# Performance work log

Hardware: AMD Instinct MI355X
Metric: run time of the kernel (lower is better)

Reference implementation:

```python
import jax, jax.numpy as jnp
import numpy as np

NUM_EXPERTS = 8
TOP_K = 2
HIDDEN = 1024
INTER = 4096
STD = 0.02


def setup_inputs() -> dict:
    key = jax.random.key(0)
    k0, k1, k2, k3 = jax.random.split(key, 4)
    hidden_states = jax.random.normal(k0, (2, 2048, HIDDEN), dtype=jnp.float32)
    gate_w = jax.random.normal(k1, (NUM_EXPERTS, HIDDEN), dtype=jnp.float32) * (HIDDEN ** -0.5)
    w1 = jax.random.normal(k2, (NUM_EXPERTS, INTER, HIDDEN), dtype=jnp.float32) * STD  # c_fc.weight
    w2 = jax.random.normal(k3, (NUM_EXPERTS, HIDDEN, INTER), dtype=jnp.float32) * STD  # c_proj.weight
    return {"hidden_states": hidden_states, "gate_w": gate_w, "w1": w1, "w2": w2}


def reference(hidden_states, gate_w, w1, w2):
    B, S, H = hidden_states.shape
    x = hidden_states.reshape(-1, H)                      # [T, H]
    T = x.shape[0]
    # ---- routing ----
    router_logits = x @ gate_w.T                          # [T, E]
    top_vals, top_idx = jax.lax.top_k(router_logits, TOP_K)
    router_weights = jax.nn.softmax(top_vals.astype(jnp.float32), axis=-1).astype(x.dtype)
    # dense combine matrix with exactly top_k nonzeros per row (math-equivalent
    # to the sort/grouped-GEMM/scatter-combine pipeline in the torch module)
    combine = jnp.zeros((T, NUM_EXPERTS), x.dtype).at[
        jnp.arange(T)[:, None], top_idx
    ].set(router_weights)                                 # [T, E]
    # ---- experts ----
    h = jax.nn.gelu(jnp.einsum('th,eih->eti', x, w1), approximate=False)  # [E, T, I]
    y = jnp.einsum('eti,ehi->eth', h, w2)                 # [E, T, H]
    out = jnp.einsum('eth,te->th', y, combine)            # weighted combine
    return out.reshape(B, S, H), router_logits
```

## Files before the change

kernel.cpp:

```cpp
#include <hip/hip_runtime.h>

#define T 4096
#define Hdim 1024
#define Idim 4096
#define NE 8
#define OUT0 4194304
#define SPLITK 2
#define BK 64

#define SLOT_CAP 9216

#define W1B_OFF 0u
#define W2B_OFF 67108864u
#define XB_OFF  134217728u
#define HB_OFF  142606336u
#define YB_OFF  218103808u
#define META_OFF 255852544u
#define M_COUNTS 0
#define M_CURS   8
#define M_OFFS   16
#define M_TEXP   32
#define M_TSLOT  8224
#define M_STOK   16416
#define M_TWF    25632

typedef short bf16x8 __attribute__((ext_vector_type(8)));
typedef float f32x4  __attribute__((ext_vector_type(4)));

__device__ __forceinline__ unsigned short f2bf(float f) {
    unsigned int b = __float_as_uint(f);
    b += 0x7fffu + ((b >> 16) & 1u);
    return (unsigned short)(b >> 16);
}
__device__ __forceinline__ float bf2f(unsigned short s) {
    return __uint_as_float(((unsigned int)s) << 16);
}

#define GLD(gsrc, ldst) \
    __builtin_amdgcn_global_load_lds( \
        (const __attribute__((address_space(1))) unsigned int*)(gsrc), \
        (__attribute__((address_space(3))) unsigned int*)(ldst), 16, 0, 0)

__global__ void cvt_w_k(const float* __restrict__ w1, const float* __restrict__ w2,
                        unsigned short* __restrict__ w1b, unsigned short* __restrict__ w2b,
                        int n4each, int* __restrict__ meta) {
    int i = blockIdx.x * blockDim.x + threadIdx.x;
    if (i < 16) meta[M_COUNTS + i] = 0;
    if (i < SLOT_CAP) meta[M_STOK + i] = -1;
    const float4* src; ushort4* dst; int j;
    if (i < n4each) { src = (const float4*)w1; dst = (ushort4*)w1b; j = i; }
    else            { src = (const float4*)w2; dst = (ushort4*)w2b; j = i - n4each; }
    float4 v = src[j];
    ushort4 o;
    o.x = f2bf(v.x); o.y = f2bf(v.y); o.z = f2bf(v.z); o.w = f2bf(v.w);
    dst[j] = o;
}

__global__ void router_k(const float* __restrict__ x, const float* __restrict__ gw,
                         float* __restrict__ logits_out, int* __restrict__ texp,
                         float* __restrict__ twf, int* __restrict__ counts,
                         unsigned short* __restrict__ xb) {
    int wv = threadIdx.x >> 6, lane = threadIdx.x & 63;
    int t = blockIdx.x * 4 + wv;
    const float* xp = x + (size_t)t * Hdim;
    unsigned short* xbp = xb + (size_t)t * Hdim;
    float s[NE];
    #pragma unroll
    for (int e = 0; e < NE; e++) s[e] = 0.f;
    #pragma unroll
    for (int j = 0; j < 16; j++) {
        float xv = xp[lane + 64 * j];
        xbp[lane + 64 * j] = f2bf(xv);
        #pragma unroll
        for (int e = 0; e < NE; e++) s[e] += xv * gw[e * Hdim + lane + 64 * j];
    }
    #pragma unroll
    for (int e = 0; e < NE; e++) {
        #pragma unroll
        for (int off = 32; off > 0; off >>= 1) s[e] += __shfl_xor(s[e], off);
    }
    if (lane == 0) {
        #pragma unroll
        for (int e = 0; e < NE; e++) logits_out[t * NE + e] = s[e];
        int i0 = 0; float v0 = s[0];
        #pragma unroll
        for (int e = 1; e < NE; e++) if (s[e] > v0) { v0 = s[e]; i0 = e; }
        int i1 = -1; float v1 = -3.4e38f;
        #pragma unroll
        for (int e = 0; e < NE; e++) if (e != i0 && s[e] > v1) { v1 = s[e]; i1 = e; }
        float e1 = expf(v1 - v0);
        float inv = 1.f / (1.f + e1);
        texp[2 * t] = i0; texp[2 * t + 1] = i1;
        twf[2 * t] = inv; twf[2 * t + 1] = e1 * inv;
        atomicAdd(&counts[i0], 1);
        atomicAdd(&counts[i1], 1);
    }
}

__global__ void assign_k(const int* __restrict__ texp, const int* __restrict__ counts,
                         int* __restrict__ curs, int* __restrict__ stok, int* __restrict__ tslot) {
    int p = blockIdx.x * blockDim.x + threadIdx.x;
    int e = texp[p];
    int off = 0;
    #pragma unroll
    for (int q = 0; q < NE; q++) {
        int pc = (counts[q] + 127) & ~127;
        off += (q < e) ? pc : 0;
    }
    int slot = off + atomicAdd(&curs[e], 1);
    stok[slot] = p >> 1;
    tslot[p] = slot;
}

__global__ __launch_bounds__(256, 3) void gemm1_k(
    const unsigned short* __restrict__ xb, const unsigned short* __restrict__ w1b,
    const int* __restrict__ counts, const int* __restrict__ stok,
    unsigned short* __restrict__ hb) {
    __shared__ __align__(16) unsigned short As[128 * BK];
    __shared__ __align__(16) unsigned short Bs[128 * BK];
    const int rt = blockIdx.y, ct = blockIdx.x;
    const int row0 = rt * 128;
    int offs[NE + 1];
    offs[0] = 0;
    #pragma unroll
    for (int q = 0; q < NE; q++) offs[q + 1] = offs[q] + ((counts[q] + 127) & ~127);
    if (row0 >= offs[NE]) return;
    int e = 0;
    #pragma unroll
    for (int q = 1; q < NE; q++) if (offs[q] <= row0) e = q;

    const int tid = threadIdx.x;
    const int lane = tid & 63, wv = tid >> 6;
    const int srow = lane >> 3;
    const int schunk = (lane & 7) ^ srow;

    const unsigned short* gA[4];
    const unsigned short* gB[4];
    unsigned short* lA[4];
    unsigned short* lB[4];
    #pragma unroll
    for (int g = 0; g < 4; g++) {
        int r = wv * 32 + g * 8 + srow;
        int t = stok[row0 + r]; if (t < 0) t = 0;
        gA[g] = xb + (size_t)t * Hdim + schunk * 8;
        gB[g] = w1b + ((size_t)e * Idim + ct * 128 + r) * Hdim + schunk * 8;
        lA[g] = As + (wv * 32 + g * 8) * BK;
        lB[g] = Bs + (wv * 32 + g * 8) * BK;
    }

    f32x4 acc[4][4] = {};
    const int mrow = (wv & 1) * 64, ncol = (wv >> 1) * 64;
    const int fr = lane & 15, qd = lane >> 4;

    const int NIT = Hdim / BK;
    for (int it = 0; it < NIT; it++) {
        #pragma unroll
        for (int g = 0; g < 4; g++) {
            GLD(gA[g] + it * BK, lA[g]);
            GLD(gB[g] + it * BK, lB[g]);
        }
        __syncthreads();
        #pragma unroll
        for (int ko = 0; ko < 2; ko++) {
            bf16x8 af[4], bff[4];
            #pragma unroll
            for (int mi = 0; mi < 4; mi++)
                af[mi]  = *(const bf16x8*)&As[(mrow + mi * 16 + fr) * BK + ((((ko << 2) | qd) ^ (fr & 7)) << 3)];
            #pragma unroll
            for (int ni = 0; ni < 4; ni++)
                bff[ni] = *(const bf16x8*)&Bs[(ncol + ni * 16 + fr) * BK + ((((ko << 2) | qd) ^ (fr & 7)) << 3)];
            #pragma unroll
            for (int mi = 0; mi < 4; mi++)
                #pragma unroll
                for (int ni = 0; ni < 4; ni++)
                    acc[mi][ni] = __builtin_amdgcn_mfma_f32_16x16x32_bf16(af[mi], bff[ni], acc[mi][ni], 0, 0, 0);
        }
        __syncthreads();
    }
    #pragma unroll
    for (int mi = 0; mi < 4; mi++) {
        #pragma unroll
        for (int ni = 0; ni < 4; ni++) {
            #pragma unroll
            for (int r = 0; r < 4; r++) {
                int row = row0 + mrow + mi * 16 + qd * 4 + r;
                int col = ct * 128 + ncol + ni * 16 + fr;
                float v = acc[mi][ni][r];
                float u = v * (1.f + 0.044715f * v * v);
                float g = v / (1.f + __expf(-1.5957691216f * u));
                hb[(size_t)row * Idim + col] = f2bf(g);
            }
        }
    }
}

__global__ __launch_bounds__(256, 3) void gemm2_k(
    const unsigned short* __restrict__ hb, const unsigned short* __restrict__ w2b,
    const int* __restrict__ counts, unsigned short* __restrict__ y16) {
    __shared__ __align__(16) unsigned short As[128 * BK];
    __shared__ __align__(16) unsigned short Bs[128 * BK];
    const int id = blockIdx.x;
    const int k8 = id & 7;
    const int j  = id >> 3;
    const int ct = j & 7;
    const int j8 = j >> 3;
    const int rtL = j8 % 9, kz = j8 / 9;
    const int rt = k8 * 9 + rtL;
    const int row0 = rt * 128;
    int offs[NE + 1];
    offs[0] = 0;
    #pragma unroll
    for (int q = 0; q < NE; q++) offs[q + 1] = offs[q] + ((counts[q] + 127) & ~127);
    if (row0 >= offs[NE]) return;
    int e = 0;
    #pragma unroll
    for (int q = 1; q < NE; q++) if (offs[q] <= row0) e = q;

    const int tid = threadIdx.x;
    const int lane = tid & 63, wv = tid >> 6;
    const int srow = lane >> 3;
    const int schunk = (lane & 7) ^ srow;

    const unsigned short* gA[4];
    const unsigned short* gB[4];
    unsigned short* lA[4];
    unsigned short* lB[4];
    #pragma unroll
    for (int g = 0; g < 4; g++) {
        int r = wv * 32 + g * 8 + srow;
        gA[g] = hb + (size_t)(row0 + r) * Idim + schunk * 8;
        gB[g] = w2b + ((size_t)e * Hdim + ct * 128 + r) * Idim + schunk * 8;
        lA[g] = As + (wv * 32 + g * 8) * BK;
        lB[g] = Bs + (wv * 32 + g * 8) * BK;
    }

    f32x4 acc[4][4] = {};
    const int mrow = (wv & 1) * 64, ncol = (wv >> 1) * 64;
    const int fr = lane & 15, qd = lane >> 4;

    const int k0 = kz * (Idim / SPLITK);
    const int NIT = (Idim / SPLITK) / BK;
    for (int it = 0; it < NIT; it++) {
        #pragma unroll
        for (int g = 0; g < 4; g++) {
            GLD(gA[g] + k0 + it * BK, lA[g]);
            GLD(gB[g] + k0 + it * BK, lB[g]);
        }
        __syncthreads();
        #pragma unroll
        for (int ko = 0; ko < 2; ko++) {
            bf16x8 af[4], bff[4];
            #pragma unroll
            for (int mi = 0; mi < 4; mi++)
                af[mi]  = *(const bf16x8*)&As[(mrow + mi * 16 + fr) * BK + ((((ko << 2) | qd) ^ (fr & 7)) << 3)];
            #pragma unroll
            for (int ni = 0; ni < 4; ni++)
                bff[ni] = *(const bf16x8*)&Bs[(ncol + ni * 16 + fr) * BK + ((((ko << 2) | qd) ^ (fr & 7)) << 3)];
            #pragma unroll
            for (int mi = 0; mi < 4; mi++)
                #pragma unroll
                for (int ni = 0; ni < 4; ni++)
                    acc[mi][ni] = __builtin_amdgcn_mfma_f32_16x16x32_bf16(af[mi], bff[ni], acc[mi][ni], 0, 0, 0);
        }
        __syncthreads();
    }
    unsigned short* yk = y16 + (size_t)kz * SLOT_CAP * Hdim;
    #pragma unroll
    for (int mi = 0; mi < 4; mi++) {
        #pragma unroll
        for (int ni = 0; ni < 4; ni++) {
            #pragma unroll
            for (int r = 0; r < 4; r++) {
                int row = row0 + mrow + mi * 16 + qd * 4 + r;
                int col = ct * 128 + ncol + ni * 16 + fr;
                yk[(size_t)row * Hdim + col] = f2bf(acc[mi][ni][r]);
            }
        }
    }
}

__global__ void combine_k(const unsigned short* __restrict__ y16, const int* __restrict__ tslot,
                          const float* __restrict__ twf, float* __restrict__ out) {
    int i = blockIdx.x * blockDim.x + threadIdx.x;
    int t = i >> 7, rem = i & 127;
    int s0 = tslot[2 * t], s1 = tslot[2 * t + 1];
    float w0 = twf[2 * t], w1 = twf[2 * t + 1];
    const uint4* y0 = (const uint4*)(y16);
    const uint4* y1 = (const uint4*)(y16 + (size_t)SLOT_CAP * Hdim);
    uint4 a0 = y0[(size_t)s0 * 128 + rem];
    uint4 a1 = y1[(size_t)s0 * 128 + rem];
    uint4 b0 = y0[(size_t)s1 * 128 + rem];
    uint4 b1 = y1[(size_t)s1 * 128 + rem];
    float o[8];
    #pragma unroll
    for (int j = 0; j < 4; j++) {
        unsigned int ua0 = ((const unsigned int*)&a0)[j], ua1 = ((const unsigned int*)&a1)[j];
        unsigned int ub0 = ((const unsigned int*)&b0)[j], ub1 = ((const unsigned int*)&b1)[j];
        float alo = bf2f((unsigned short)ua0) + bf2f((unsigned short)ua1);
        float ahi = bf2f((unsigned short)(ua0 >> 16)) + bf2f((unsigned short)(ua1 >> 16));
        float blo = bf2f((unsigned short)ub0) + bf2f((unsigned short)ub1);
        float bhi = bf2f((unsigned short)(ub0 >> 16)) + bf2f((unsigned short)(ub1 >> 16));
        o[2 * j]     = w0 * alo + w1 * blo;
        o[2 * j + 1] = w0 * ahi + w1 * bhi;
    }
    float4* out4 = (float4*)out;
    out4[2 * i]     = make_float4(o[0], o[1], o[2], o[3]);
    out4[2 * i + 1] = make_float4(o[4], o[5], o[6], o[7]);
}

extern "C" void kernel_launch(void* const* d_in, const int* in_sizes, int n_in,
                              void* d_out, int out_size, void* d_ws, size_t ws_size,
                              hipStream_t stream) {
    const float* x  = (const float*)d_in[0];
    const float* gw = (const float*)d_in[1];
    const float* w1 = (const float*)d_in[2];
    const float* w2 = (const float*)d_in[3];
    float* out = (float*)d_out;

    char* ws = (char*)d_ws;
    unsigned short* w1b = (unsigned short*)(ws + W1B_OFF);
    unsigned short* w2b = (unsigned short*)(ws + W2B_OFF);
    unsigned short* xb  = (unsigned short*)(ws + XB_OFF);
    unsigned short* hb  = (unsigned short*)(ws + HB_OFF);
    unsigned short* y16 = (unsigned short*)(ws + YB_OFF);
    int*            meta = (int*)(ws + META_OFF);
    int* counts = meta + M_COUNTS;
    int* curs   = meta + M_CURS;
    int* texp   = meta + M_TEXP;
    int* tslot  = meta + M_TSLOT;
    int* stok   = meta + M_STOK;
    float* twf  = (float*)(meta + M_TWF);

    cvt_w_k<<<65536, 256, 0, stream>>>(w1, w2, w1b, w2b, NE * Idim * Hdim / 4, meta);
    router_k<<<T / 4, 256, 0, stream>>>(x, gw, out + OUT0, texp, twf, counts, xb);
    assign_k<<<32, 256, 0, stream>>>(texp, counts, curs, stok, tslot);
    gemm1_k<<<dim3(Idim / 128, SLOT_CAP / 128), 256, 0, stream>>>(xb, w1b, counts, stok, hb);
    gemm2_k<<<(Hdim / 128) * (SLOT_CAP / 128) * SPLITK, 256, 0, stream>>>(hb, w2b, counts, y16);
    combine_k<<<T * Hdim / 8 / 256, 256, 0, stream>>>(y16, tslot, twf, out);
}
```

Measured before the change: 618.1 us.

## Fuse weighted combine into gemm2 epilogue via atomic adds, raise split-K to 4

```diff
diff --git a/kernel.cpp b/kernel.cpp
--- a/kernel.cpp
+++ b/kernel.cpp
@@ -5,7 +5,7 @@
 #define Idim 4096
 #define NE 8
 #define OUT0 4194304
-#define SPLITK 2
+#define SPLITK 4
 #define BK 64
 
 #define SLOT_CAP 9216
@@ -14,15 +14,14 @@
 #define W2B_OFF 67108864u
 #define XB_OFF  134217728u
 #define HB_OFF  142606336u
-#define YB_OFF  218103808u
-#define META_OFF 255852544u
+#define META_OFF 218103808u
 #define M_COUNTS 0
 #define M_CURS   8
-#define M_OFFS   16
 #define M_TEXP   32
 #define M_TSLOT  8224
 #define M_STOK   16416
 #define M_TWF    25632
+#define M_SWF    33824
 
 typedef short bf16x8 __attribute__((ext_vector_type(8)));
 typedef float f32x4  __attribute__((ext_vector_type(4)));
@@ -43,10 +42,14 @@
 
 __global__ void cvt_w_k(const float* __restrict__ w1, const float* __restrict__ w2,
                         unsigned short* __restrict__ w1b, unsigned short* __restrict__ w2b,
-                        int n4each, int* __restrict__ meta) {
+                        int n4each, int* __restrict__ meta, float* __restrict__ out) {
     int i = blockIdx.x * blockDim.x + threadIdx.x;
     if (i < 16) meta[M_COUNTS + i] = 0;
-    if (i < SLOT_CAP) meta[M_STOK + i] = -1;
+    if (i < SLOT_CAP) {
+        meta[M_STOK + i] = -1;
+        ((float*)(meta + M_SWF))[i] = 0.f;
+    }
+    if (i < T * Hdim / 4) ((float4*)out)[i] = make_float4(0.f, 0.f, 0.f, 0.f);
     const float4* src; ushort4* dst; int j;
     if (i < n4each) { src = (const float4*)w1; dst = (ushort4*)w1b; j = i; }
     else            { src = (const float4*)w2; dst = (ushort4*)w2b; j = i - n4each; }
@@ -98,7 +101,9 @@
 }
 
 __global__ void assign_k(const int* __restrict__ texp, const int* __restrict__ counts,
-                         int* __restrict__ curs, int* __restrict__ stok, int* __restrict__ tslot) {
+                         const float* __restrict__ twf, int* __restrict__ curs,
+                         int* __restrict__ stok, int* __restrict__ tslot,
+                         float* __restrict__ swf) {
     int p = blockIdx.x * blockDim.x + threadIdx.x;
     int e = texp[p];
     int off = 0;
@@ -109,6 +114,7 @@
     }
     int slot = off + atomicAdd(&curs[e], 1);
     stok[slot] = p >> 1;
+    swf[slot] = twf[p];
     tslot[p] = slot;
 }
 
@@ -196,7 +202,8 @@
 
 __global__ __launch_bounds__(256, 3) void gemm2_k(
     const unsigned short* __restrict__ hb, const unsigned short* __restrict__ w2b,
-    const int* __restrict__ counts, unsigned short* __restrict__ y16) {
+    const int* __restrict__ counts, const int* __restrict__ stok,
+    const float* __restrict__ swf, float* __restrict__ out) {
     __shared__ __align__(16) unsigned short As[128 * BK];
     __shared__ __align__(16) unsigned short Bs[128 * BK];
     const int id = blockIdx.x;
@@ -264,48 +271,21 @@
         }
         __syncthreads();
     }
-    unsigned short* yk = y16 + (size_t)kz * SLOT_CAP * Hdim;
     #pragma unroll
     for (int mi = 0; mi < 4; mi++) {
         #pragma unroll
-        for (int ni = 0; ni < 4; ni++) {
-            #pragma unroll
-            for (int r = 0; r < 4; r++) {
-                int row = row0 + mrow + mi * 16 + qd * 4 + r;
-                int col = ct * 128 + ncol + ni * 16 + fr;
-                yk[(size_t)row * Hdim + col] = f2bf(acc[mi][ni][r]);
+        for (int r = 0; r < 4; r++) {
+            int row = row0 + mrow + mi * 16 + qd * 4 + r;
+            int tk = stok[row];
+            float w = swf[row];
+            if (tk >= 0) {
+                float* op = out + (size_t)tk * Hdim + ct * 128 + ncol + fr;
+                #pragma unroll
+                for (int ni = 0; ni < 4; ni++)
+                    atomicAdd(op + ni * 16, w * acc[mi][ni][r]);
             }
         }
     }
-}
-
-__global__ void combine_k(const unsigned short* __restrict__ y16, const int* __restrict__ tslot,
-                          const float* __restrict__ twf, float* __restrict__ out) {
-    int i = blockIdx.x * blockDim.x + threadIdx.x;
-    int t = i >> 7, rem = i & 127;
-    int s0 = tslot[2 * t], s1 = tslot[2 * t + 1];
-    float w0 = twf[2 * t], w1 = twf[2 * t + 1];
-    const uint4* y0 = (const uint4*)(y16);
-    const uint4* y1 = (const uint4*)(y16 + (size_t)SLOT_CAP * Hdim);
-    uint4 a0 = y0[(size_t)s0 * 128 + rem];
-    uint4 a1 = y1[(size_t)s0 * 128 + rem];
-    uint4 b0 = y0[(size_t)s1 * 128 + rem];
-    uint4 b1 = y1[(size_t)s1 * 128 + rem];
-    float o[8];
-    #pragma unroll
-    for (int j = 0; j < 4; j++) {
-        unsigned int ua0 = ((const unsigned int*)&a0)[j], ua1 = ((const unsigned int*)&a1)[j];
-        unsigned int ub0 = ((const unsigned int*)&b0)[j], ub1 = ((const unsigned int*)&b1)[j];
-        float alo = bf2f((unsigned short)ua0) + bf2f((unsigned short)ua1);
-        float ahi = bf2f((unsigned short)(ua0 >> 16)) + bf2f((unsigned short)(ua1 >> 16));
-        float blo = bf2f((unsigned short)ub0) + bf2f((unsigned short)ub1);
-        float bhi = bf2f((unsigned short)(ub0 >> 16)) + bf2f((unsigned short)(ub1 >> 16));
-        o[2 * j]     = w0 * alo + w1 * blo;
-        o[2 * j + 1] = w0 * ahi + w1 * bhi;
-    }
-    float4* out4 = (float4*)out;
-    out4[2 * i]     = make_float4(o[0], o[1], o[2], o[3]);
-    out4[2 * i + 1] = make_float4(o[4], o[5], o[6], o[7]);
 }
 
 extern "C" void kernel_launch(void* const* d_in, const int* in_sizes, int n_in,
@@ -322,7 +302,6 @@
     unsigned short* w2b = (unsigned short*)(ws + W2B_OFF);
     unsigned short* xb  = (unsigned short*)(ws + XB_OFF);
     unsigned short* hb  = (unsigned short*)(ws + HB_OFF);
-    unsigned short* y16 = (unsigned short*)(ws + YB_OFF);
     int*            meta = (int*)(ws + META_OFF);
     int* counts = meta + M_COUNTS;
     int* curs   = meta + M_CURS;
@@ -330,11 +309,11 @@
     int* tslot  = meta + M_TSLOT;
     int* stok   = meta + M_STOK;
     float* twf  = (float*)(meta + M_TWF);
-
-    cvt_w_k<<<65536, 256, 0, stream>>>(w1, w2, w1b, w2b, NE * Idim * Hdim / 4, meta);
+    float* swf  = (float*)(meta + M_SWF);
+
+    cvt_w_k<<<65536, 256, 0, stream>>>(w1, w2, w1b, w2b, NE * Idim * Hdim / 4, meta, out);
     router_k<<<T / 4, 256, 0, stream>>>(x, gw, out + OUT0, texp, twf, counts, xb);
-    assign_k<<<32, 256, 0, stream>>>(texp, counts, curs, stok, tslot);
+    assign_k<<<32, 256, 0, stream>>>(texp, counts, twf, curs, stok, tslot, swf);
     gemm1_k<<<dim3(Idim / 128, SLOT_CAP / 128), 256, 0, stream>>>(xb, w1b, counts, stok, hb);
-    gemm2_k<<<(Hdim / 128) * (SLOT_CAP / 128) * SPLITK, 256, 0, stream>>>(hb, w2b, counts, y16);
-    combine_k<<<T * Hdim / 8 / 256, 256, 0, stream>>>(y16, tslot, twf, out);
-}
+    gemm2_k<<<(Hdim / 128) * (SLOT_CAP / 128) * SPLITK, 256, 0, stream>>>(hb, w2b, counts, stok, swf, out);
+}
```

Result: slower. 668.7 us (+8.2%).

## Fuse fp32-to-bf16 weight conversion into GEMM B-tile loads with register prefetch

Applied to the files above, without the earlier changes.

```diff
diff --git a/kernel.cpp b/kernel.cpp
--- a/kernel.cpp
+++ b/kernel.cpp
@@ -10,15 +10,12 @@
 
 #define SLOT_CAP 9216
 
-#define W1B_OFF 0u
-#define W2B_OFF 67108864u
-#define XB_OFF  134217728u
-#define HB_OFF  142606336u
-#define YB_OFF  218103808u
-#define META_OFF 255852544u
+#define XB_OFF  0u
+#define HB_OFF  8388608u
+#define YB_OFF  83886080u
+#define META_OFF 121634816u
 #define M_COUNTS 0
 #define M_CURS   8
-#define M_OFFS   16
 #define M_TEXP   32
 #define M_TSLOT  8224
 #define M_STOK   16416
@@ -41,19 +38,10 @@
         (const __attribute__((address_space(1))) unsigned int*)(gsrc), \
         (__attribute__((address_space(3))) unsigned int*)(ldst), 16, 0, 0)
 
-__global__ void cvt_w_k(const float* __restrict__ w1, const float* __restrict__ w2,
-                        unsigned short* __restrict__ w1b, unsigned short* __restrict__ w2b,
-                        int n4each, int* __restrict__ meta) {
+__global__ void zero_k(int* meta) {
     int i = blockIdx.x * blockDim.x + threadIdx.x;
     if (i < 16) meta[M_COUNTS + i] = 0;
     if (i < SLOT_CAP) meta[M_STOK + i] = -1;
-    const float4* src; ushort4* dst; int j;
-    if (i < n4each) { src = (const float4*)w1; dst = (ushort4*)w1b; j = i; }
-    else            { src = (const float4*)w2; dst = (ushort4*)w2b; j = i - n4each; }
-    float4 v = src[j];
-    ushort4 o;
-    o.x = f2bf(v.x); o.y = f2bf(v.y); o.z = f2bf(v.z); o.w = f2bf(v.w);
-    dst[j] = o;
 }
 
 __global__ void router_k(const float* __restrict__ x, const float* __restrict__ gw,
@@ -112,8 +100,24 @@
     tslot[p] = slot;
 }
 
+#define LOADB(off) \
+    b00 = *(const float4*)(gB0 + (off)); b01 = *(const float4*)(gB0 + (off) + 4); \
+    b10 = *(const float4*)(gB1 + (off)); b11 = *(const float4*)(gB1 + (off) + 4); \
+    b20 = *(const float4*)(gB2 + (off)); b21 = *(const float4*)(gB2 + (off) + 4); \
+    b30 = *(const float4*)(gB3 + (off)); b31 = *(const float4*)(gB3 + (off) + 4);
+#define PK2(lo, hi) (((unsigned)f2bf(lo)) | (((unsigned)f2bf(hi)) << 16))
+#define CVTSTOREB() { uint4 q; \
+    q.x = PK2(b00.x, b00.y); q.y = PK2(b00.z, b00.w); \
+    q.z = PK2(b01.x, b01.y); q.w = PK2(b01.z, b01.w); *(uint4*)lb0 = q; \
+    q.x = PK2(b10.x, b10.y); q.y = PK2(b10.z, b10.w); \
+    q.z = PK2(b11.x, b11.y); q.w = PK2(b11.z, b11.w); *(uint4*)lb1 = q; \
+    q.x = PK2(b20.x, b20.y); q.y = PK2(b20.z, b20.w); \
+    q.z = PK2(b21.x, b21.y); q.w = PK2(b21.z, b21.w); *(uint4*)lb2 = q; \
+    q.x = PK2(b30.x, b30.y); q.y = PK2(b30.z, b30.w); \
+    q.z = PK2(b31.x, b31.y); q.w = PK2(b31.z, b31.w); *(uint4*)lb3 = q; }
+
 __global__ __launch_bounds__(256, 3) void gemm1_k(
-    const unsigned short* __restrict__ xb, const unsigned short* __restrict__ w1b,
+    const unsigned short* __restrict__ xb, const float* __restrict__ w1,
     const int* __restrict__ counts, const int* __restrict__ stok,
     unsigned short* __restrict__ hb) {
     __shared__ __align__(16) unsigned short As[128 * BK];
@@ -135,31 +139,39 @@
     const int schunk = (lane & 7) ^ srow;
 
     const unsigned short* gA[4];
-    const unsigned short* gB[4];
     unsigned short* lA[4];
-    unsigned short* lB[4];
     #pragma unroll
     for (int g = 0; g < 4; g++) {
         int r = wv * 32 + g * 8 + srow;
         int t = stok[row0 + r]; if (t < 0) t = 0;
         gA[g] = xb + (size_t)t * Hdim + schunk * 8;
-        gB[g] = w1b + ((size_t)e * Idim + ct * 128 + r) * Hdim + schunk * 8;
         lA[g] = As + (wv * 32 + g * 8) * BK;
-        lB[g] = Bs + (wv * 32 + g * 8) * BK;
-    }
+    }
+    int rB0 = wv * 32 + 0 * 8 + srow, rB1 = wv * 32 + 1 * 8 + srow;
+    int rB2 = wv * 32 + 2 * 8 + srow, rB3 = wv * 32 + 3 * 8 + srow;
+    const float* gB0 = w1 + ((size_t)e * Idim + ct * 128 + rB0) * Hdim + schunk * 8;
+    const float* gB1 = w1 + ((size_t)e * Idim + ct * 128 + rB1) * Hdim + schunk * 8;
+    const float* gB2 = w1 + ((size_t)e * Idim + ct * 128 + rB2) * Hdim + schunk * 8;
+    const float* gB3 = w1 + ((size_t)e * Idim + ct * 128 + rB3) * Hdim + schunk * 8;
+    unsigned short* lb0 = Bs + (wv * 32 + 0 * 8) * BK + lane * 8;
+    unsigned short* lb1 = Bs + (wv * 32 + 1 * 8) * BK + lane * 8;
+    unsigned short* lb2 = Bs + (wv * 32 + 2 * 8) * BK + lane * 8;
+    unsigned short* lb3 = Bs + (wv * 32 + 3 * 8) * BK + lane * 8;
 
     f32x4 acc[4][4] = {};
     const int mrow = (wv & 1) * 64, ncol = (wv >> 1) * 64;
     const int fr = lane & 15, qd = lane >> 4;
 
+    float4 b00, b01, b10, b11, b20, b21, b30, b31;
+    #pragma unroll
+    for (int g = 0; g < 4; g++) GLD(gA[g], lA[g]);
+    LOADB(0)
+    CVTSTOREB()
+    __syncthreads();
+
     const int NIT = Hdim / BK;
     for (int it = 0; it < NIT; it++) {
-        #pragma unroll
-        for (int g = 0; g < 4; g++) {
-            GLD(gA[g] + it * BK, lA[g]);
-            GLD(gB[g] + it * BK, lB[g]);
-        }
-        __syncthreads();
+        if (it + 1 < NIT) { LOADB((it + 1) * BK) }
         #pragma unroll
         for (int ko = 0; ko < 2; ko++) {
             bf16x8 af[4], bff[4];
@@ -175,7 +187,13 @@
                 for (int ni = 0; ni < 4; ni++)
                     acc[mi][ni] = __builtin_amdgcn_mfma_f32_16x16x32_bf16(af[mi], bff[ni], acc[mi][ni], 0, 0, 0);
         }
-        __syncthreads();
+        if (it + 1 < NIT) {
+            __syncthreads();
+            #pragma unroll
+            for (int g = 0; g < 4; g++) GLD(gA[g] + (it + 1) * BK, lA[g]);
+            CVTSTOREB()
+            __syncthreads();
+        }
     }
     #pragma unroll
     for (int mi = 0; mi < 4; mi++) {
@@ -195,7 +213,7 @@
 }
 
 __global__ __launch_bounds__(256, 3) void gemm2_k(
-    const unsigned short* __restrict__ hb, const unsigned short* __restrict__ w2b,
+    const unsigned short* __restrict__ hb, const float* __restrict__ w2,
     const int* __restrict__ counts, unsigned short* __restrict__ y16) {
     __shared__ __align__(16) unsigned short As[128 * BK];
     __shared__ __align__(16) unsigned short Bs[128 * BK];
@@ -222,31 +240,39 @@
     const int schunk = (lane & 7) ^ srow;
 
     const unsigned short* gA[4];
-    const unsigned short* gB[4];
     unsigned short* lA[4];
-    unsigned short* lB[4];
     #pragma unroll
     for (int g = 0; g < 4; g++) {
         int r = wv * 32 + g * 8 + srow;
         gA[g] = hb + (size_t)(row0 + r) * Idim + schunk * 8;
-        gB[g] = w2b + ((size_t)e * Hdim + ct * 128 + r) * Idim + schunk * 8;
         lA[g] = As + (wv * 32 + g * 8) * BK;
-        lB[g] = Bs + (wv * 32 + g * 8) * BK;
-    }
+    }
+    int rB0 = wv * 32 + 0 * 8 + srow, rB1 = wv * 32 + 1 * 8 + srow;
+    int rB2 = wv * 32 + 2 * 8 + srow, rB3 = wv * 32 + 3 * 8 + srow;
+    const float* gB0 = w2 + ((size_t)e * Hdim + ct * 128 + rB0) * Idim + schunk * 8;
+    const float* gB1 = w2 + ((size_t)e * Hdim + ct * 128 + rB1) * Idim + schunk * 8;
+    const float* gB2 = w2 + ((size_t)e * Hdim + ct * 128 + rB2) * Idim + schunk * 8;
+    const float* gB3 = w2 + ((size_t)e * Hdim + ct * 128 + rB3) * Idim + schunk * 8;
+    unsigned short* lb0 = Bs + (wv * 32 + 0 * 8) * BK + lane * 8;
+    unsigned short* lb1 = Bs + (wv * 32 + 1 * 8) * BK + lane * 8;
+    unsigned short* lb2 = Bs + (wv * 32 + 2 * 8) * BK + lane * 8;
+    unsigned short* lb3 = Bs + (wv * 32 + 3 * 8) * BK + lane * 8;
 
     f32x4 acc[4][4] = {};
     const int mrow = (wv & 1) * 64, ncol = (wv >> 1) * 64;
     const int fr = lane & 15, qd = lane >> 4;
 
     const int k0 = kz * (Idim / SPLITK);
+    float4 b00, b01, b10, b11, b20, b21, b30, b31;
+    #pragma unroll
+    for (int g = 0; g < 4; g++) GLD(gA[g] + k0, lA[g]);
+    LOADB(k0)
+    CVTSTOREB()
+    __syncthreads();
+
     const int NIT = (Idim / SPLITK) / BK;
     for (int it = 0; it < NIT; it++) {
-        #pragma unroll
-        for (int g = 0; g < 4; g++) {
-            GLD(gA[g] + k0 + it * BK, lA[g]);
-            GLD(gB[g] + k0 + it * BK, lB[g]);
-        }
-        __syncthreads();
+        if (it + 1 < NIT) { LOADB(k0 + (it + 1) * BK) }
         #pragma unroll
         for (int ko = 0; ko < 2; ko++) {
             bf16x8 af[4], bff[4];
@@ -262,7 +288,13 @@
                 for (int ni = 0; ni < 4; ni++)
                     acc[mi][ni] = __builtin_amdgcn_mfma_f32_16x16x32_bf16(af[mi], bff[ni], acc[mi][ni], 0, 0, 0);
         }
-        __syncthreads();
+        if (it + 1 < NIT) {
+            __syncthreads();
+            #pragma unroll
+            for (int g = 0; g < 4; g++) GLD(gA[g] + k0 + (it + 1) * BK, lA[g]);
+            CVTSTOREB()
+            __syncthreads();
+        }
     }
     unsigned short* yk = y16 + (size_t)kz * SLOT_CAP * Hdim;
     #pragma unroll
@@ -318,8 +350,6 @@
     float* out = (float*)d_out;
 
     char* ws = (char*)d_ws;
-    unsigned short* w1b = (unsigned short*)(ws + W1B_OFF);
-    unsigned short* w2b = (unsigned short*)(ws + W2B_OFF);
     unsigned short* xb  = (unsigned short*)(ws + XB_OFF);
     unsigned short* hb  = (unsigned short*)(ws + HB_OFF);
     unsigned short* y16 = (unsigned short*)(ws + YB_OFF);
@@ -331,10 +361,10 @@
     int* stok   = meta + M_STOK;
     float* twf  = (float*)(meta + M_TWF);
 
-    cvt_w_k<<<65536, 256, 0, stream>>>(w1, w2, w1b, w2b, NE * Idim * Hdim / 4, meta);
+    zero_k<<<36, 256, 0, stream>>>(meta);
     router_k<<<T / 4, 256, 0, stream>>>(x, gw, out + OUT0, texp, twf, counts, xb);
     assign_k<<<32, 256, 0, stream>>>(texp, counts, curs, stok, tslot);
-    gemm1_k<<<dim3(Idim / 128, SLOT_CAP / 128), 256, 0, stream>>>(xb, w1b, counts, stok, hb);
-    gemm2_k<<<(Hdim / 128) * (SLOT_CAP / 128) * SPLITK, 256, 0, stream>>>(hb, w2b, counts, y16);
+    gemm1_k<<<dim3(Idim / 128, SLOT_CAP / 128), 256, 0, stream>>>(xb, w1, counts, stok, hb);
+    gemm2_k<<<(Hdim / 128) * (SLOT_CAP / 128) * SPLITK, 256, 0, stream>>>(hb, w2, counts, y16);
     combine_k<<<T * Hdim / 8 / 256, 256, 0, stream>>>(y16, tslot, twf, out);
 }
```

After: 630.8 us. 2.0% more time.

## Remap gemm1 blocks per XCD and raise gemm2 split-K to four

Applied to the files above, without the earlier changes.

```diff
diff --git a/kernel.cpp b/kernel.cpp
--- a/kernel.cpp
+++ b/kernel.cpp
@@ -5,20 +5,20 @@
 #define Idim 4096
 #define NE 8
 #define OUT0 4194304
-#define SPLITK 2
+#define SPLITK 4
 #define BK 64
 
 #define SLOT_CAP 9216
 
 #define W1B_OFF 0u
-#define W2B_OFF 67108864u
-#define XB_OFF  134217728u
+#define XB_OFF  67108864u
+#define W2B_OFF 75497472u
 #define HB_OFF  142606336u
-#define YB_OFF  218103808u
+#define YA_OFF  218103808u
+#define YB_OFF  0u
 #define META_OFF 255852544u
 #define M_COUNTS 0
 #define M_CURS   8
-#define M_OFFS   16
 #define M_TEXP   32
 #define M_TSLOT  8224
 #define M_STOK   16416
@@ -118,7 +118,12 @@
     unsigned short* __restrict__ hb) {
     __shared__ __align__(16) unsigned short As[128 * BK];
     __shared__ __align__(16) unsigned short Bs[128 * BK];
-    const int rt = blockIdx.y, ct = blockIdx.x;
+    const int id = blockIdx.x;
+    const int k8 = id & 7;
+    const int j  = id >> 3;
+    const int ct = j & 31;
+    const int rtL = j >> 5;
+    const int rt = k8 * 9 + rtL;
     const int row0 = rt * 128;
     int offs[NE + 1];
     offs[0] = 0;
@@ -196,7 +201,8 @@
 
 __global__ __launch_bounds__(256, 3) void gemm2_k(
     const unsigned short* __restrict__ hb, const unsigned short* __restrict__ w2b,
-    const int* __restrict__ counts, unsigned short* __restrict__ y16) {
+    const int* __restrict__ counts, unsigned short* __restrict__ ya,
+    unsigned short* __restrict__ yb) {
     __shared__ __align__(16) unsigned short As[128 * BK];
     __shared__ __align__(16) unsigned short Bs[128 * BK];
     const int id = blockIdx.x;
@@ -264,7 +270,8 @@
         }
         __syncthreads();
     }
-    unsigned short* yk = y16 + (size_t)kz * SLOT_CAP * Hdim;
+    unsigned short* yk = (kz < 2) ? (ya + (size_t)kz * SLOT_CAP * Hdim)
+                                  : (yb + (size_t)(kz - 2) * SLOT_CAP * Hdim);
     #pragma unroll
     for (int mi = 0; mi < 4; mi++) {
         #pragma unroll
@@ -279,27 +286,40 @@
     }
 }
 
-__global__ void combine_k(const unsigned short* __restrict__ y16, const int* __restrict__ tslot,
-                          const float* __restrict__ twf, float* __restrict__ out) {
+__global__ void combine_k(const unsigned short* __restrict__ ya, const unsigned short* __restrict__ yb,
+                          const int* __restrict__ tslot, const float* __restrict__ twf,
+                          float* __restrict__ out) {
     int i = blockIdx.x * blockDim.x + threadIdx.x;
     int t = i >> 7, rem = i & 127;
     int s0 = tslot[2 * t], s1 = tslot[2 * t + 1];
     float w0 = twf[2 * t], w1 = twf[2 * t + 1];
-    const uint4* y0 = (const uint4*)(y16);
-    const uint4* y1 = (const uint4*)(y16 + (size_t)SLOT_CAP * Hdim);
+    const uint4* y0 = (const uint4*)(ya);
+    const uint4* y1 = (const uint4*)(ya + (size_t)SLOT_CAP * Hdim);
+    const uint4* y2 = (const uint4*)(yb);
+    const uint4* y3 = (const uint4*)(yb + (size_t)SLOT_CAP * Hdim);
     uint4 a0 = y0[(size_t)s0 * 128 + rem];
     uint4 a1 = y1[(size_t)s0 * 128 + rem];
+    uint4 a2 = y2[(size_t)s0 * 128 + rem];
+    uint4 a3 = y3[(size_t)s0 * 128 + rem];
     uint4 b0 = y0[(size_t)s1 * 128 + rem];
     uint4 b1 = y1[(size_t)s1 * 128 + rem];
+    uint4 b2 = y2[(size_t)s1 * 128 + rem];
+    uint4 b3 = y3[(size_t)s1 * 128 + rem];
     float o[8];
     #pragma unroll
     for (int j = 0; j < 4; j++) {
         unsigned int ua0 = ((const unsigned int*)&a0)[j], ua1 = ((const unsigned int*)&a1)[j];
+        unsigned int ua2 = ((const unsigned int*)&a2)[j], ua3 = ((const unsigned int*)&a3)[j];
         unsigned int ub0 = ((const unsigned int*)&b0)[j], ub1 = ((const unsigned int*)&b1)[j];
-        float alo = bf2f((unsigned short)ua0) + bf2f((unsigned short)ua1);
-        float ahi = bf2f((unsigned short)(ua0 >> 16)) + bf2f((unsigned short)(ua1 >> 16));
-        float blo = bf2f((unsigned short)ub0) + bf2f((unsigned short)ub1);
-        float bhi = bf2f((unsigned short)(ub0 >> 16)) + bf2f((unsigned short)(ub1 >> 16));
+        unsigned int ub2 = ((const unsigned int*)&b2)[j], ub3 = ((const unsigned int*)&b3)[j];
+        float alo = (bf2f((unsigned short)ua0) + bf2f((unsigned short)ua1))
+                  + (bf2f((unsigned short)ua2) + bf2f((unsigned short)ua3));
+        float ahi = (bf2f((unsigned short)(ua0 >> 16)) + bf2f((unsigned short)(ua1 >> 16)))
+                  + (bf2f((unsigned short)(ua2 >> 16)) + bf2f((unsigned short)(ua3 >> 16)));
+        float blo = (bf2f((unsigned short)ub0) + bf2f((unsigned short)ub1))
+                  + (bf2f((unsigned short)ub2) + bf2f((unsigned short)ub3));
+        float bhi = (bf2f((unsigned short)(ub0 >> 16)) + bf2f((unsigned short)(ub1 >> 16)))
+                  + (bf2f((unsigned short)(ub2 >> 16)) + bf2f((unsigned short)(ub3 >> 16)));
         o[2 * j]     = w0 * alo + w1 * blo;
         o[2 * j + 1] = w0 * ahi + w1 * bhi;
     }
@@ -322,7 +342,8 @@
     unsigned short* w2b = (unsigned short*)(ws + W2B_OFF);
     unsigned short* xb  = (unsigned short*)(ws + XB_OFF);
     unsigned short* hb  = (unsigned short*)(ws + HB_OFF);
-    unsigned short* y16 = (unsigned short*)(ws + YB_OFF);
+    unsigned short* ya  = (unsigned short*)(ws + YA_OFF);
+    unsigned short* yb  = (unsigned short*)(ws + YB_OFF);
     int*            meta = (int*)(ws + META_OFF);
     int* counts = meta + M_COUNTS;
     int* curs   = meta + M_CURS;
@@ -334,7 +355,7 @@
     cvt_w_k<<<65536, 256, 0, stream>>>(w1, w2, w1b, w2b, NE * Idim * Hdim / 4, meta);
     router_k<<<T / 4, 256, 0, stream>>>(x, gw, out + OUT0, texp, twf, counts, xb);
     assign_k<<<32, 256, 0, stream>>>(texp, counts, curs, stok, tslot);
-    gemm1_k<<<dim3(Idim / 128, SLOT_CAP / 128), 256, 0, stream>>>(xb, w1b, counts, stok, hb);
-    gemm2_k<<<(Hdim / 128) * (SLOT_CAP / 128) * SPLITK, 256, 0, stream>>>(hb, w2b, counts, y16);
-    combine_k<<<T * Hdim / 8 / 256, 256, 0, stream>>>(y16, tslot, twf, out);
-}
+    gemm1_k<<<2304, 256, 0, stream>>>(xb, w1b, counts, stok, hb);
+    gemm2_k<<<(Hdim / 128) * (SLOT_CAP / 128) * SPLITK, 256, 0, stream>>>(hb, w2b, counts, ya, yb);
+    combine_k<<<T * Hdim / 8 / 256, 256, 0, stream>>>(ya, yb, tslot, twf, out);
+}
```

Result: no change. 616.9 us (-0.2%).
